# Kernel tuning notes

Measured on AMD Instinct MI355X. Metric: run time of the kernel, lower is better.

## Reference

```python
import jax, jax.numpy as jnp
import numpy as np

HIDDEN = 128
K = 20
T = 20000
N_PTS = 10011


def setup_inputs() -> dict:
    key = jax.random.key(0)
    ks = jax.random.split(key, 20)
    points = jax.random.normal(ks[0], (N_PTS, 3), dtype=jnp.float32)
    triangles = jax.random.randint(ks[1], (T, 3), 0, N_PTS, dtype=jnp.int64)
    init_probs = jax.random.uniform(ks[2], (T,), dtype=jnp.float32)
    s = 0.05
    inp = {"points": points, "triangles": triangles, "init_probs": init_probs}
    for li in range(3):
        inp[f"W1_{li}"] = jax.random.normal(ks[3 + 4 * li], (HIDDEN, HIDDEN + 9), dtype=jnp.float32) * s
        inp[f"b1_{li}"] = jnp.zeros((HIDDEN,), dtype=jnp.float32)
        inp[f"W2_{li}"] = jax.random.normal(ks[4 + 4 * li], (HIDDEN, HIDDEN), dtype=jnp.float32) * s
        inp[f"b2_{li}"] = jnp.zeros((HIDDEN,), dtype=jnp.float32)
    inp["Wf"] = jax.random.normal(ks[15], (1, HIDDEN), dtype=jnp.float32) * s
    inp["bf"] = jnp.zeros((1,), dtype=jnp.float32)
    return inp


def _geometry(points, triangles):
    tp = points[triangles]                      # [T, 3verts, 3xyz]
    e_ij = tp[:, 0] - tp[:, 1]
    e_ik = tp[:, 0] - tp[:, 2]
    e_jk = tp[:, 1] - tp[:, 2]
    ev = jnp.stack([e_ij, e_ik, e_jk], axis=1)  # [T, 3, 3]
    t_max = jnp.max(ev, axis=1)                 # [T, 3]
    t_min = jnp.min(ev, axis=1)                 # [T, 3]
    bary = tp.mean(axis=1)                      # [T, 3]
    return t_min, t_max, bary


def _knn_edges(bary, k):
    # squared distances (monotone in cdist) -> same k smallest neighbors
    sq = jnp.sum(bary * bary, axis=1)
    d2 = sq[:, None] + sq[None, :] - 2.0 * (bary @ bary.T)   # [T, T]
    _, idx = jax.lax.top_k(-d2, k + 1)                       # k+1 smallest
    nbr = idx[:, 1:]                                         # drop self
    t = bary.shape[0]
    src = jnp.repeat(jnp.arange(t, dtype=nbr.dtype), k)      # [T*k]
    tgt = nbr.reshape(-1)                                    # [T*k]
    return src, tgt


def _triconv(x, t_min, t_max, bary, src, tgt, W1, b1, W2, b2):
    r_n_k = jnp.concatenate(
        [t_min[src] - t_min[tgt], t_max[src] - t_max[tgt], bary[src] - bary[tgt]],
        axis=1,
    )                                                        # [E, 9]
    h = jnp.concatenate([r_n_k, x[src] - x[tgt]], axis=1)    # [E, H+9]
    h = jax.nn.relu(h @ W1.T + b1) @ W2.T + b2               # [E, H]
    return jax.ops.segment_sum(h, src, num_segments=x.shape[0])


def reference(points, triangles, init_probs,
              W1_0, b1_0, W2_0, b2_0,
              W1_1, b1_1, W2_1, b2_1,
              W1_2, b1_2, W2_2, b2_2,
              Wf, bf):
    t_min, t_max, bary = _geometry(points, triangles)
    k = min(K, triangles.shape[0] - 1)
    src, tgt = _knn_edges(bary, k)
    feats = jnp.broadcast_to(init_probs[:, None], (init_probs.shape[0], HIDDEN))
    feats = _triconv(feats, t_min, t_max, bary, src, tgt, W1_0, b1_0, W2_0, b2_0)
    feats = _triconv(feats, t_min, t_max, bary, src, tgt, W1_1, b1_1, W2_1, b2_1)
    feats = _triconv(feats, t_min, t_max, bary, src, tgt, W1_2, b1_2, W2_2, b2_2)
    logits = (feats @ Wf.T + bf)[:, 0]
    return jax.nn.sigmoid(logits)
```

## Files before the change

### kernel.cpp

```cpp
#include <hip/hip_runtime.h>
#include <math.h>

#define T_TRI 20000
#define KNN_K 20
#define H     128

#define WS_GEO    0
#define WS_BQ     (1u<<20)
#define WS_NBR    (2u<<20)
#define WS_RS     (4u<<20)
#define WS_MT     ((4u<<20)+4096)
#define WS_WV     ((4u<<20)+4096+(256u<<10))
#define WS_MM     (5u<<20)
#define WS_CSTART ((5u<<20)+64)
#define WS_CPTR   ((5u<<20)+(32u<<10))
#define WS_HIST   ((5u<<20)+(64u<<10))
#define WS_CID    ((5u<<20)+(128u<<10))
#define WS_CSORT  ((5u<<20)+(256u<<10))
#define WS_OID    ((5u<<20)+(384u<<10))
#define WS_BQS    ((5u<<20)+(512u<<10))
#define WS_WA     ((5u<<20)+(840u<<10))
#define WS_PS     (6u<<20)
#define WS_GEOS   (7u<<20)
#define WS_ZB     (9u<<20)
#define WS_ZA     (20u<<20)

__device__ __forceinline__ float readlane_f(float v, int l) {
    return __uint_as_float(__builtin_amdgcn_readlane(__float_as_uint(v), l));
}
__device__ __forceinline__ unsigned encf(float f) {
    unsigned u = __float_as_uint(f);
    return (u & 0x80000000u) ? ~u : (u | 0x80000000u);
}
__device__ __forceinline__ float decf(unsigned e) {
    unsigned u = (e & 0x80000000u) ? (e & 0x7FFFFFFFu) : ~e;
    return __uint_as_float(u);
}
__device__ __forceinline__ int xcd_swz(int bid, int nwg) {
    int q = nwg >> 3, rm = nwg & 7;
    int x = bid & 7, idx = bid >> 3;
    return (x < rm) ? x*(q+1) + idx : rm*(q+1) + (x-rm)*q + idx;
}

__global__ void grid_init_kernel(unsigned* __restrict__ hist, unsigned* __restrict__ mm) {
    int i = blockIdx.x * 256 + threadIdx.x;
    if (i < 4096) hist[i] = 0u;
    if (i < 3) mm[i] = 0xFFFFFFFFu;
    if (i >= 3 && i < 6) mm[i] = 0u;
}

__global__ void geom_kernel(const float* __restrict__ pts, const int* __restrict__ tris,
                            float* __restrict__ geo, float4* __restrict__ bq,
                            unsigned* __restrict__ mm) {
    int t = blockIdx.x * blockDim.x + threadIdx.x;
    int lane = threadIdx.x & 63;
    bool act = (t < T_TRI);
    int tt = act ? t : 0;
    int i0 = tris[3*tt], i1 = tris[3*tt+1], i2 = tris[3*tt+2];
    float ax = pts[3*i0], ay = pts[3*i0+1], az = pts[3*i0+2];
    float bx = pts[3*i1], by = pts[3*i1+1], bz = pts[3*i1+2];
    float cx = pts[3*i2], cy = pts[3*i2+1], cz = pts[3*i2+2];
    float e0x = ax-bx, e0y = ay-by, e0z = az-bz;
    float e1x = ax-cx, e1y = ay-cy, e1z = az-cz;
    float e2x = bx-cx, e2y = by-cy, e2z = bz-cz;
    float mnx = fminf(fminf(e0x,e1x),e2x), mny = fminf(fminf(e0y,e1y),e2y), mnz = fminf(fminf(e0z,e1z),e2z);
    float mxx = fmaxf(fmaxf(e0x,e1x),e2x), mxy = fmaxf(fmaxf(e0y,e1y),e2y), mxz = fmaxf(fmaxf(e0z,e1z),e2z);
    float gx = (ax+bx+cx)*(1.0f/3.0f), gy = (ay+by+cy)*(1.0f/3.0f), gz = (az+bz+cz)*(1.0f/3.0f);
    float sq = (gx*gx + gy*gy) + gz*gz;
    if (act) {
        float* g = geo + (size_t)t*12;
        g[0]=mnx; g[1]=mny; g[2]=mnz; g[3]=mxx; g[4]=mxy; g[5]=mxz;
        g[6]=gx;  g[7]=gy;  g[8]=gz;  g[9]=0.f; g[10]=0.f; g[11]=0.f;
        bq[t] = make_float4(gx, gy, gz, sq);
    }
    unsigned n0 = act ? encf(gx) : 0xFFFFFFFFu;
    unsigned n1 = act ? encf(gy) : 0xFFFFFFFFu;
    unsigned n2 = act ? encf(gz) : 0xFFFFFFFFu;
    unsigned x0 = act ? encf(gx) : 0u;
    unsigned x1 = act ? encf(gy) : 0u;
    unsigned x2 = act ? encf(gz) : 0u;
#pragma unroll
    for (int off = 32; off >= 1; off >>= 1) {
        n0 = min(n0, (unsigned)__shfl_xor((int)n0, off));
        n1 = min(n1, (unsigned)__shfl_xor((int)n1, off));
        n2 = min(n2, (unsigned)__shfl_xor((int)n2, off));
        x0 = max(x0, (unsigned)__shfl_xor((int)x0, off));
        x1 = max(x1, (unsigned)__shfl_xor((int)x1, off));
        x2 = max(x2, (unsigned)__shfl_xor((int)x2, off));
    }
    if (lane == 0) {
        atomicMin(&mm[0], n0); atomicMin(&mm[1], n1); atomicMin(&mm[2], n2);
        atomicMax(&mm[3], x0); atomicMax(&mm[4], x1); atomicMax(&mm[5], x2);
    }
}

__global__ void cellhist_kernel(const float4* __restrict__ bq, const unsigned* __restrict__ mm,
                                int* __restrict__ cellid, unsigned* __restrict__ hist) {
    int t = blockIdx.x * 256 + threadIdx.x;
    if (t >= T_TRI) return;
    float mnx = decf(mm[0]), mny = decf(mm[1]), mnz = decf(mm[2]);
    float mxx = decf(mm[3]), mxy = decf(mm[4]), mxz = decf(mm[5]);
    float ihx = 16.f / fmaxf(mxx-mnx, 1e-30f);
    float ihy = 16.f / fmaxf(mxy-mny, 1e-30f);
    float ihz = 16.f / fmaxf(mxz-mnz, 1e-30f);
    float4 b = bq[t];
    int ix = min(15, max(0, (int)((b.x-mnx)*ihx)));
    int iy = min(15, max(0, (int)((b.y-mny)*ihy)));
    int iz = min(15, max(0, (int)((b.z-mnz)*ihz)));
    int c = (ix<<8) | (iy<<4) | iz;
    cellid[t] = c;
    atomicAdd(&hist[c], 1u);
}

__global__ __launch_bounds__(1024) void prefix_kernel(const unsigned* __restrict__ hist,
                                                      unsigned* __restrict__ cellstart,
                                                      unsigned* __restrict__ cellptr) {
    __shared__ unsigned sbuf[1024];
    int tid = threadIdx.x;
    uint4 v = ((const uint4*)hist)[tid];
    unsigned mysum = v.x + v.y + v.z + v.w;
    sbuf[tid] = mysum;
    __syncthreads();
    for (int off = 1; off < 1024; off <<= 1) {
        unsigned add = (tid >= off) ? sbuf[tid - off] : 0u;
        __syncthreads();
        sbuf[tid] += add;
        __syncthreads();
    }
    unsigned excl = sbuf[tid] - mysum;
    unsigned p0 = excl, p1 = p0 + v.x, p2 = p1 + v.y, p3 = p2 + v.z;
    cellstart[4*tid+0] = p0; cellstart[4*tid+1] = p1;
    cellstart[4*tid+2] = p2; cellstart[4*tid+3] = p3;
    cellptr[4*tid+0] = p0; cellptr[4*tid+1] = p1;
    cellptr[4*tid+2] = p2; cellptr[4*tid+3] = p3;
    if (tid == 1023) cellstart[4096] = p3 + v.w;
}

__global__ void scatter_kernel(const float4* __restrict__ bq, const int* __restrict__ cellid,
                               const float* __restrict__ geo, const float* __restrict__ probs,
                               unsigned* __restrict__ cellptr, float4* __restrict__ bqs,
                               int* __restrict__ oid, int* __restrict__ csort,
                               float* __restrict__ geo_s, float* __restrict__ probs_s) {
    int t = blockIdx.x * 256 + threadIdx.x;
    if (t >= T_TRI) return;
    int c = cellid[t];
    unsigned p = atomicAdd(&cellptr[c], 1u);
    bqs[p] = bq[t];
    oid[p]  = t;
    csort[p] = c;
    const float4* g4 = (const float4*)geo;
    float4* g4s = (float4*)geo_s;
    g4s[(size_t)p*3+0] = g4[(size_t)t*3+0];
    g4s[(size_t)p*3+1] = g4[(size_t)t*3+1];
    g4s[(size_t)p*3+2] = g4[(size_t)t*3+2];
    probs_s[p] = probs[t];
}

__global__ __launch_bounds__(256) void knn_grid_kernel(const float4* __restrict__ bqs,
        const int* __restrict__ oid, const int* __restrict__ csort,
        const unsigned* __restrict__ cellstart, const unsigned* __restrict__ mm,
        int* __restrict__ nbr) {
    int wave = threadIdx.x >> 6, lane = threadIdx.x & 63;
    int r = blockIdx.x * 4 + wave;
    float4 q = bqs[r];
    int myc = csort[r];
    int cx = (myc>>8)&15, cy = (myc>>4)&15, cz = myc&15;
    float mnx = decf(mm[0]), mny = decf(mm[1]), mnz = decf(mm[2]);
    float hx = (decf(mm[3]) - mnx) * (1.f/16.f);
    float hy = (decf(mm[4]) - mny) * (1.f/16.f);
    float hz = (decf(mm[5]) - mnz) * (1.f/16.f);
    float hmin = fminf(hx, fminf(hy, hz));

    float rd = INFINITY;
    int   ri = 0x7FF00000 | lane;
    int   rk = lane;
    float th = INFINITY;
    int   mi = 0x7FFFFFFF;

#define SCAN_RANGE(RS, RE)                                                          \
    for (unsigned base = (RS); base < (RE); base += 64u) {                          \
        unsigned k = base + (unsigned)lane;                                         \
        bool kv = (k < (RE));                                                       \
        float4 c4 = kv ? bqs[k] : make_float4(INFINITY,INFINITY,INFINITY,INFINITY); \
        int ov = kv ? oid[k] : 0x7FFFFFFF;                                          \
        float dot = fmaf(q.z, c4.z, fmaf(q.y, c4.y, q.x*c4.x));                     \
        float d = (q.w + c4.w) - 2.0f*dot;                                          \
        unsigned long long bal = __ballot(kv && (d <= th));                         \
        while (bal) {                                                               \
            int src = __ffsll(bal) - 1; bal &= bal - 1;                             \
            float dc = readlane_f(d, src);                                          \
            int   jc = __builtin_amdgcn_readlane(ov, src);                          \
            int   kc = (int)base + src;                                             \
            if ((dc < th) || (dc == th && jc < mi)) {                               \
                bool less = (rd < dc) || (rd == dc && ri < jc);                     \
                int pos = __popcll(__ballot(less) & 0x1FFFFFull);                   \
                float sd = __shfl_up(rd, 1);                                        \
                int   si = __shfl_up(ri, 1);                                        \
                int   sk = __shfl_up(rk, 1);                                        \
                if (lane < 21) {                                                    \
                    if (lane == pos)      { rd = dc; ri = jc; rk = kc; }            \
                    else if (lane > pos)  { rd = sd; ri = si; rk = sk; }            \
                }                                                                   \
                th = readlane_f(rd, 20);                                            \
                mi = __builtin_amdgcn_readlane(ri, 20);                             \
            }                                                                       \
        }                                                                           \
    }

#define CELL_BOUND_OK(EX, EY, EZ)                                                   \
    ({  float cl0 = fmaf((float)(EX), hx, mnx);                                     \
        float cm0 = fmaf((float)(EY), hy, mny);                                     \
        float cn0 = fmaf((float)(EZ), hz, mnz);                                     \
        float ddx = fmaxf(fmaxf(cl0 - q.x, q.x - (cl0 + hx)), 0.f);                 \
        float ddy = fmaxf(fmaxf(cm0 - q.y, q.y - (cm0 + hy)), 0.f);                 \
        float ddz = fmaxf(fmaxf(cn0 - q.z, q.z - (cn0 + hz)), 0.f);                 \
        float bnd = fmaf(ddx, ddx, fmaf(ddy, ddy, ddz*ddz));                        \
        (bnd <= th + 1e-3f); })

    {
        unsigned hs = cellstart[myc], he = cellstart[myc + 1];
        SCAN_RANGE(hs, he)
    }

    for (int w = 1; w <= 15; ++w) {
        if (w == 1) {
            int i = lane;
            bool val = (i < 27) && (i != 13);
            int ii = (i < 27) ? i : 0;
            int dz = ii % 3 - 1, dy = (ii / 3) % 3 - 1, dx = ii / 9 - 1;
            int ex = cx + dx, ey = cy + dy, ez = cz + dz;
            val = val && ex >= 0 && ex < 16 && ey >= 0 && ey < 16 && ez >= 0 && ez < 16;
            int cell = (ex<<8) | (ey<<4) | ez;
            unsigned cs = 0u, ce = 0u;
            if (val) { cs = cellstart[cell]; ce = cellstart[cell+1]; }
            val = val && (cs < ce);
            if (val) val = CELL_BOUND_OK(ex, ey, ez);
            unsigned long long cm = __ballot(val);
            while (cm) {
                int cl = __ffsll(cm) - 1; cm &= cm - 1;
                unsigned s0 = (unsigned)__builtin_amdgcn_readlane((int)cs, cl);
                unsigned e0 = (unsigned)__builtin_amdgcn_readlane((int)ce, cl);
                SCAN_RANGE(s0, e0)
            }
        } else {
            int W = 2*w + 1, W2 = W*W, tot = W*W2;
            for (int b0 = 0; b0 < tot; b0 += 64) {
                int i = b0 + lane;
                bool val = (i < tot);
                int ii = val ? i : 0;
                int dz = ii % W - w, dy = (ii / W) % W - w, dx = ii / W2 - w;
                int cheb = max(abs(dx), max(abs(dy), abs(dz)));
                val = val && (cheb == w);
                int ex = cx + dx, ey = cy + dy, ez = cz + dz;
                val = val && ex >= 0 && ex < 16 && ey >= 0 && ey < 16 && ez >= 0 && ez < 16;
                int cell = (ex<<8) | (ey<<4) | ez;
                unsigned cs = 0u, ce = 0u;
                if (val) { cs = cellstart[cell]; ce = cellstart[cell+1]; }
                val = val && (cs < ce);
                if (val) val = CELL_BOUND_OK(ex, ey, ez);
                unsigned long long cm = __ballot(val);
                while (cm) {
                    int cl = __ffsll(cm) - 1; cm &= cm - 1;
                    unsigned s0 = (unsigned)__builtin_amdgcn_readlane((int)cs, cl);
                    unsigned e0 = (unsigned)__builtin_amdgcn_readlane((int)ce, cl);
                    SCAN_RANGE(s0, e0)
                }
            }
        }
        bool covered = (cx-w <= 0) && (cx+w >= 15) && (cy-w <= 0) && (cy+w >= 15)
                    && (cz-w <= 0) && (cz+w >= 15);
        if (covered) break;
        float bd = (float)w * hmin - 1e-3f;
        if (bd > 0.f && th < bd*bd) break;
    }
#undef CELL_BOUND_OK
#undef SCAN_RANGE
    if (lane >= 1 && lane < 21) nbr[r*KNN_K + lane - 1] = rk;
}

__global__ void rowsum_kernel(const float* __restrict__ W1, float* __restrict__ rs) {
    int f = threadIdx.x;
    float s = 0.f;
    for (int c = 0; c < H; ++c) s += W1[f*137 + 9 + c];
    rs[f] = s;
}
__global__ void watrans_kernel(const float* __restrict__ W10, const float* __restrict__ W11,
                               const float* __restrict__ W12, float* __restrict__ WA) {
    int f = threadIdx.x, c = blockIdx.x, m = blockIdx.y;
    const float* W = (m == 0) ? W10 : (m == 1) ? W11 : W12;
    WA[m*9*128 + c*128 + f] = W[f*137 + c];
}

__global__ void mfold_kernel(const float* __restrict__ W11, const float* __restrict__ W12,
                             const float* __restrict__ W20, const float* __restrict__ W21,
                             float* __restrict__ MTg) {
    int c = threadIdx.x, f = blockIdx.x, m = blockIdx.y;
    const float* W1 = m ? W12 : W11;
    const float* W2 = m ? W21 : W20;
    float acc = 0.f;
    for (int k = 0; k < 128; ++k)
        acc = fmaf(W1[f*137 + 9 + k], W2[k*128 + c], acc);
    MTg[m*16384 + (c>>2)*512 + f*4 + (c&3)] = acc;
}
__global__ void vhead_kernel(const float* __restrict__ W11, const float* __restrict__ W12,
                             const float* __restrict__ b20, const float* __restrict__ b21,
                             const float* __restrict__ b22, const float* __restrict__ W22,
                             const float* __restrict__ Wf, const float* __restrict__ bf,
                             float* __restrict__ WV) {
    int f = threadIdx.x;
    float v0 = 0.f, v1 = 0.f, w2 = 0.f;
    for (int k = 0; k < 128; ++k) {
        v0 = fmaf(W11[f*137 + 9 + k], b20[k], v0);
        v1 = fmaf(W12[f*137 + 9 + k], b21[k], v1);
        w2 = fmaf(Wf[k], W22[k*128 + f], w2);
    }
    WV[f]       = (float)KNN_K * v0;
    WV[128 + f] = (float)KNN_K * v1;
    WV[256 + f] = w2;
    if (f == 0) {
        float cacc = 0.f;
        for (int k = 0; k < 128; ++k) cacc = fmaf(Wf[k], b22[k], cacc);
        WV[384] = (float)KNN_K * cacc + bf[0];
    }
}

__global__ void y0_kernel(const float* __restrict__ ps, const float* __restrict__ rs,
                          const float* __restrict__ WA0, const float* __restrict__ geo_s,
                          float* __restrict__ Z) {
    int bid = xcd_swz(blockIdx.x, gridDim.x);
    int tid = bid * 256 + threadIdx.x;
    int t = tid >> 7, f = tid & 127;
    float acc = ps[t] * rs[f];
#pragma unroll
    for (int c = 0; c < 9; ++c)
        acc = fmaf(WA0[c*128 + f], geo_s[(size_t)t*12 + c], acc);
    Z[tid] = acc;
}

__global__ __launch_bounds__(256) void ef_mid_kernel(const float* __restrict__ Z,
                            const int* __restrict__ nbr, const float* __restrict__ b1,
                            const float* __restrict__ MTg, const float* __restrict__ v,
                            const float* __restrict__ WAn, const float* __restrict__ geo_s,
                            float* __restrict__ Znext) {
    __shared__ float Srow[4][128];
    int wave = threadIdx.x >> 6, lane = threadIdx.x & 63;
    int t0b = xcd_swz(blockIdx.x, gridDim.x) * 4;
    {
        int t = t0b + wave;
        float zsLo = Z[(size_t)t*H + lane]      + b1[lane];
        float zsHi = Z[(size_t)t*H + 64 + lane] + b1[64 + lane];
        float accLo = 0.f, accHi = 0.f;
#pragma unroll
        for (int e = 0; e < KNN_K; ++e) {
            int tg = nbr[t*KNN_K + e];
            accLo += fmaxf(zsLo - Z[(size_t)tg*H + lane],      0.f);
            accHi += fmaxf(zsHi - Z[(size_t)tg*H + 64 + lane], 0.f);
        }
        Srow[wave][lane]    = accLo;
        Srow[wave][64+lane] = accHi;
    }
    __syncthreads();
    int f = threadIdx.x & 127, half = threadIdx.x >> 7;
    float a0 = v[f], a1 = v[f];
    const int r0_ = half * 2;
#pragma unroll
    for (int c4 = 0; c4 < 32; ++c4) {
        float4 w = *(const float4*)&MTg[c4*512 + f*4];
        float4 v0 = ((const float4*)Srow[r0_+0])[c4];
        float4 v1 = ((const float4*)Srow[r0_+1])[c4];
        a0 = fmaf(w.x, v0.x, a0); a0 = fmaf(w.y, v0.y, a0);
        a0 = fmaf(w.z, v0.z, a0); a0 = fmaf(w.w, v0.w, a0);
        a1 = fmaf(w.x, v1.x, a1); a1 = fmaf(w.y, v1.y, a1);
        a1 = fmaf(w.z, v1.z, a1); a1 = fmaf(w.w, v1.w, a1);
    }
#pragma unroll
    for (int c = 0; c < 9; ++c) {
        float w = WAn[c*128 + f];
        a0 = fmaf(w, geo_s[(size_t)(t0b + r0_ + 0)*12 + c], a0);
        a1 = fmaf(w, geo_s[(size_t)(t0b + r0_ + 1)*12 + c], a1);
    }
    Znext[(size_t)(t0b+r0_+0)*H + f] = a0;
    Znext[(size_t)(t0b+r0_+1)*H + f] = a1;
}

__global__ __launch_bounds__(256) void ef_head_kernel(const float* __restrict__ Z,
                            const int* __restrict__ nbr, const float* __restrict__ b1,
                            const float* __restrict__ WV, float* __restrict__ out,
                            const int* __restrict__ oid) {
    int wave = threadIdx.x >> 6, lane = threadIdx.x & 63;
    int t = xcd_swz(blockIdx.x, gridDim.x) * 4 + wave;
    float zsLo = Z[(size_t)t*H + lane]      + b1[lane];
    float zsHi = Z[(size_t)t*H + 64 + lane] + b1[64 + lane];
    float accLo = 0.f, accHi = 0.f;
#pragma unroll
    for (int e = 0; e < KNN_K; ++e) {
        int tg = nbr[t*KNN_K + e];
        accLo += fmaxf(zsLo - Z[(size_t)tg*H + lane],      0.f);
        accHi += fmaxf(zsHi - Z[(size_t)tg*H + 64 + lane], 0.f);
    }
    float p = fmaf(accLo, WV[256 + lane], accHi * WV[256 + 64 + lane]);
#pragma unroll
    for (int off = 32; off >= 1; off >>= 1) p += __shfl_xor(p, off);
    if (lane == 0) {
        float z = p + WV[384];
        out[oid[t]] = 1.0f / (1.0f + expf(-z));
    }
}

extern "C" void kernel_launch(void* const* d_in, const int* in_sizes, int n_in,
                              void* d_out, int out_size, void* d_ws, size_t ws_size,
                              hipStream_t stream) {
    (void)in_sizes; (void)n_in; (void)out_size; (void)ws_size;
    const float* pts   = (const float*)d_in[0];
    const int*   tris  = (const int*)d_in[1];
    const float* probs = (const float*)d_in[2];
    const float* W1[3] = {(const float*)d_in[3],  (const float*)d_in[7],  (const float*)d_in[11]};
    const float* b1[3] = {(const float*)d_in[4],  (const float*)d_in[8],  (const float*)d_in[12]};
    const float* W2[3] = {(const float*)d_in[5],  (const float*)d_in[9],  (const float*)d_in[13]};
    const float* b2[3] = {(const float*)d_in[6],  (const float*)d_in[10], (const float*)d_in[14]};
    const float* Wf = (const float*)d_in[15];
    const float* bf = (const float*)d_in[16];
    float* out = (float*)d_out;

    char* ws = (char*)d_ws;
    float*    geo  = (float*)(ws + WS_GEO);
    float4*   bq   = (float4*)(ws + WS_BQ);
    int*      nbr  = (int*)(ws + WS_NBR);
    float*    rs   = (float*)(ws + WS_RS);
    float*    MTg  = (float*)(ws + WS_MT);
    float*    WV   = (float*)(ws + WS_WV);
    unsigned* mm   = (unsigned*)(ws + WS_MM);
    unsigned* cst  = (unsigned*)(ws + WS_CSTART);
    unsigned* cptr = (unsigned*)(ws + WS_CPTR);
    unsigned* hist = (unsigned*)(ws + WS_HIST);
    int*      cid  = (int*)(ws + WS_CID);
    int*      cso  = (int*)(ws + WS_CSORT);
    int*      oid  = (int*)(ws + WS_OID);
    float4*   bqs  = (float4*)(ws + WS_BQS);
    float*    WA   = (float*)(ws + WS_WA);
    float*    ps   = (float*)(ws + WS_PS);
    float*    geos = (float*)(ws + WS_GEOS);
    float*    Za   = (float*)(ws + WS_ZA);
    float*    Zb   = (float*)(ws + WS_ZB);

    grid_init_kernel<<<16, 256, 0, stream>>>(hist, mm);
    geom_kernel<<<(T_TRI+255)/256, 256, 0, stream>>>(pts, tris, geo, bq, mm);
    cellhist_kernel<<<(T_TRI+255)/256, 256, 0, stream>>>(bq, mm, cid, hist);
    prefix_kernel<<<1, 1024, 0, stream>>>(hist, cst, cptr);
    scatter_kernel<<<(T_TRI+255)/256, 256, 0, stream>>>(bq, cid, geo, probs, cptr, bqs, oid, cso, geos, ps);
    knn_grid_kernel<<<T_TRI/4, 256, 0, stream>>>(bqs, oid, cso, cst, mm, nbr);
    rowsum_kernel<<<1, 128, 0, stream>>>(W1[0], rs);
    watrans_kernel<<<dim3(9,3), 128, 0, stream>>>(W1[0], W1[1], W1[2], WA);
    mfold_kernel<<<dim3(128,2), 128, 0, stream>>>(W1[1], W1[2], W2[0], W2[1], MTg);
    vhead_kernel<<<1, 128, 0, stream>>>(W1[1], W1[2], b2[0], b2[1], b2[2], W2[2], Wf, bf, WV);
    y0_kernel<<<(T_TRI*H)/256, 256, 0, stream>>>(ps, rs, WA, geos, Za);
    ef_mid_kernel<<<T_TRI/4, 256, 0, stream>>>(Za, nbr, b1[0], MTg,           WV,       WA + 1*9*128, geos, Zb);
    ef_mid_kernel<<<T_TRI/4, 256, 0, stream>>>(Zb, nbr, b1[1], MTg + 16384,   WV + 128, WA + 2*9*128, geos, Za);
    ef_head_kernel<<<T_TRI/4, 256, 0, stream>>>(Za, nbr, b1[2], WV, out, oid);
}
```

Baseline: 279.5 us.

## Bitonic-sort home cell in KNN, merge weight-prep kernels, widen ef_mid blocks

The KNN kernel now loads the first 64 candidates of the query's home cell in one shot and bitonic-sorts them across the wave to seed the top-k, instead of feeding them one at a time through the scan macro. Any remaining home-cell candidates still go through the old scan. Three small weight-preprocessing kernels are merged into one prep kernel to cut launch count. ef_mid now uses 512-thread blocks handling 8 triangles, so each MTg weight load is shared by more rows, with more LDS and register pressure per block in exchange.

```diff
diff --git a/kernel.cpp b/kernel.cpp
--- a/kernel.cpp
+++ b/kernel.cpp
@@ -219,7 +219,32 @@
 
     {
         unsigned hs = cellstart[myc], he = cellstart[myc + 1];
-        SCAN_RANGE(hs, he)
+        unsigned k64 = hs + (unsigned)lane;
+        bool kv = (k64 < he);
+        float4 c4 = kv ? bqs[k64] : make_float4(INFINITY,INFINITY,INFINITY,INFINITY);
+        float dot = fmaf(q.z, c4.z, fmaf(q.y, c4.y, q.x*c4.x));
+        float d = (q.w + c4.w) - 2.0f*dot;
+        int   jx = kv ? oid[k64] : (0x7FF00000 | lane);
+        int   kc = kv ? (int)k64 : 0;
+        if (!kv) d = INFINITY;
+#pragma unroll
+        for (int kk = 2; kk <= 64; kk <<= 1) {
+#pragma unroll
+            for (int jj = kk >> 1; jj >= 1; jj >>= 1) {
+                float od = __shfl_xor(d, jj);
+                int   oj = __shfl_xor(jx, jj);
+                int   ok = __shfl_xor(kc, jj);
+                bool up    = ((lane & kk) == 0);
+                bool lower = ((lane & jj) == 0);
+                bool less  = (d < od) || (d == od && jx < oj);
+                bool keep  = ((lower == up) ? less : !less);
+                d = keep ? d : od; jx = keep ? jx : oj; kc = keep ? kc : ok;
+            }
+        }
+        rd = d; ri = jx; rk = kc;
+        th = readlane_f(rd, 20);
+        mi = __builtin_amdgcn_readlane(ri, 20);
+        if (hs + 64u < he) { SCAN_RANGE(hs + 64u, he) }
     }
 
     for (int w = 1; w <= 15; ++w) {
@@ -278,17 +303,37 @@
     if (lane >= 1 && lane < 21) nbr[r*KNN_K + lane - 1] = rk;
 }
 
-__global__ void rowsum_kernel(const float* __restrict__ W1, float* __restrict__ rs) {
+__global__ void prep_kernel(const float* __restrict__ W10, const float* __restrict__ W11,
+                            const float* __restrict__ W12,
+                            const float* __restrict__ b20, const float* __restrict__ b21,
+                            const float* __restrict__ b22, const float* __restrict__ W22,
+                            const float* __restrict__ Wf, const float* __restrict__ bf,
+                            float* __restrict__ rs, float* __restrict__ WA,
+                            float* __restrict__ WV) {
     int f = threadIdx.x;
     float s = 0.f;
-    for (int c = 0; c < H; ++c) s += W1[f*137 + 9 + c];
+    for (int c = 0; c < H; ++c) s += W10[f*137 + 9 + c];
     rs[f] = s;
-}
-__global__ void watrans_kernel(const float* __restrict__ W10, const float* __restrict__ W11,
-                               const float* __restrict__ W12, float* __restrict__ WA) {
-    int f = threadIdx.x, c = blockIdx.x, m = blockIdx.y;
-    const float* W = (m == 0) ? W10 : (m == 1) ? W11 : W12;
-    WA[m*9*128 + c*128 + f] = W[f*137 + c];
+#pragma unroll
+    for (int c = 0; c < 9; ++c) {
+        WA[0*1152 + c*128 + f] = W10[f*137 + c];
+        WA[1*1152 + c*128 + f] = W11[f*137 + c];
+        WA[2*1152 + c*128 + f] = W12[f*137 + c];
+    }
+    float v0 = 0.f, v1 = 0.f, w2 = 0.f;
+    for (int k = 0; k < 128; ++k) {
+        v0 = fmaf(W11[f*137 + 9 + k], b20[k], v0);
+        v1 = fmaf(W12[f*137 + 9 + k], b21[k], v1);
+        w2 = fmaf(Wf[k], W22[k*128 + f], w2);
+    }
+    WV[f]       = (float)KNN_K * v0;
+    WV[128 + f] = (float)KNN_K * v1;
+    WV[256 + f] = w2;
+    if (f == 0) {
+        float cacc = 0.f;
+        for (int k = 0; k < 128; ++k) cacc = fmaf(Wf[k], b22[k], cacc);
+        WV[384] = (float)KNN_K * cacc + bf[0];
+    }
 }
 
 __global__ void mfold_kernel(const float* __restrict__ W11, const float* __restrict__ W12,
@@ -302,27 +347,6 @@
         acc = fmaf(W1[f*137 + 9 + k], W2[k*128 + c], acc);
     MTg[m*16384 + (c>>2)*512 + f*4 + (c&3)] = acc;
 }
-__global__ void vhead_kernel(const float* __restrict__ W11, const float* __restrict__ W12,
-                             const float* __restrict__ b20, const float* __restrict__ b21,
-                             const float* __restrict__ b22, const float* __restrict__ W22,
-                             const float* __restrict__ Wf, const float* __restrict__ bf,
-                             float* __restrict__ WV) {
-    int f = threadIdx.x;
-    float v0 = 0.f, v1 = 0.f, w2 = 0.f;
-    for (int k = 0; k < 128; ++k) {
-        v0 = fmaf(W11[f*137 + 9 + k], b20[k], v0);
-        v1 = fmaf(W12[f*137 + 9 + k], b21[k], v1);
-        w2 = fmaf(Wf[k], W22[k*128 + f], w2);
-    }
-    WV[f]       = (float)KNN_K * v0;
-    WV[128 + f] = (float)KNN_K * v1;
-    WV[256 + f] = w2;
-    if (f == 0) {
-        float cacc = 0.f;
-        for (int k = 0; k < 128; ++k) cacc = fmaf(Wf[k], b22[k], cacc);
-        WV[384] = (float)KNN_K * cacc + bf[0];
-    }
-}
 
 __global__ void y0_kernel(const float* __restrict__ ps, const float* __restrict__ rs,
                           const float* __restrict__ WA0, const float* __restrict__ geo_s,
@@ -337,14 +361,14 @@
     Z[tid] = acc;
 }
 
-__global__ __launch_bounds__(256) void ef_mid_kernel(const float* __restrict__ Z,
+__global__ __launch_bounds__(512) void ef_mid_kernel(const float* __restrict__ Z,
                             const int* __restrict__ nbr, const float* __restrict__ b1,
                             const float* __restrict__ MTg, const float* __restrict__ v,
                             const float* __restrict__ WAn, const float* __restrict__ geo_s,
                             float* __restrict__ Znext) {
-    __shared__ float Srow[4][128];
+    __shared__ float Srow[8][128];
     int wave = threadIdx.x >> 6, lane = threadIdx.x & 63;
-    int t0b = xcd_swz(blockIdx.x, gridDim.x) * 4;
+    int t0b = xcd_swz(blockIdx.x, gridDim.x) * 8;
     {
         int t = t0b + wave;
         float zsLo = Z[(size_t)t*H + lane]      + b1[lane];
@@ -360,9 +384,9 @@
         Srow[wave][64+lane] = accHi;
     }
     __syncthreads();
-    int f = threadIdx.x & 127, half = threadIdx.x >> 7;
+    int f = threadIdx.x & 127, grp = threadIdx.x >> 7;
     float a0 = v[f], a1 = v[f];
-    const int r0_ = half * 2;
+    const int r0_ = grp * 2;
 #pragma unroll
     for (int c4 = 0; c4 < 32; ++c4) {
         float4 w = *(const float4*)&MTg[c4*512 + f*4];
@@ -449,12 +473,10 @@
     prefix_kernel<<<1, 1024, 0, stream>>>(hist, cst, cptr);
     scatter_kernel<<<(T_TRI+255)/256, 256, 0, stream>>>(bq, cid, geo, probs, cptr, bqs, oid, cso, geos, ps);
     knn_grid_kernel<<<T_TRI/4, 256, 0, stream>>>(bqs, oid, cso, cst, mm, nbr);
-    rowsum_kernel<<<1, 128, 0, stream>>>(W1[0], rs);
-    watrans_kernel<<<dim3(9,3), 128, 0, stream>>>(W1[0], W1[1], W1[2], WA);
+    prep_kernel<<<1, 128, 0, stream>>>(W1[0], W1[1], W1[2], b2[0], b2[1], b2[2], W2[2], Wf, bf, rs, WA, WV);
     mfold_kernel<<<dim3(128,2), 128, 0, stream>>>(W1[1], W1[2], W2[0], W2[1], MTg);
-    vhead_kernel<<<1, 128, 0, stream>>>(W1[1], W1[2], b2[0], b2[1], b2[2], W2[2], Wf, bf, WV);
     y0_kernel<<<(T_TRI*H)/256, 256, 0, stream>>>(ps, rs, WA, geos, Za);
-    ef_mid_kernel<<<T_TRI/4, 256, 0, stream>>>(Za, nbr, b1[0], MTg,           WV,       WA + 1*9*128, geos, Zb);
-    ef_mid_kernel<<<T_TRI/4, 256, 0, stream>>>(Zb, nbr, b1[1], MTg + 16384,   WV + 128, WA + 2*9*128, geos, Za);
+    ef_mid_kernel<<<T_TRI/8, 512, 0, stream>>>(Za, nbr, b1[0], MTg,         WV,       WA + 1*1152, geos, Zb);
+    ef_mid_kernel<<<T_TRI/8, 512, 0, stream>>>(Zb, nbr, b1[1], MTg + 16384, WV + 128, WA + 2*1152, geos, Za);
     ef_head_kernel<<<T_TRI/4, 256, 0, stream>>>(Za, nbr, b1[2], WV, out, oid);
 }
```

After: 251.6 us. 10.0% less time.
